# Optimization experiments

Hardware: AMD Instinct MI355X
Metric: run time of the kernel (lower is better)

The kernel has to match this reference:

```python
import jax, jax.numpy as jnp
import numpy as np

N = 100000

def gcn_conv(x, edge_index, W, b):
    # PyG GCNConv: add self-loops, symmetric norm D^-1/2 (A+I) D^-1/2, then aggregate x@W
    n = x.shape[0]
    loops = jnp.arange(n, dtype=edge_index.dtype)
    row = jnp.concatenate([edge_index[0], loops])  # source
    col = jnp.concatenate([edge_index[1], loops])  # target
    deg = jax.ops.segment_sum(jnp.ones_like(col, dtype=x.dtype), col, num_segments=n)
    dinv = jnp.where(deg > 0, jax.lax.rsqrt(deg), 0.0)
    norm = dinv[row] * dinv[col]            # [E+N]
    xw = x @ W                               # transform first (smaller message dim)
    msg = xw[row] * norm[:, None]            # gather + normalize
    out = jax.ops.segment_sum(msg, col, num_segments=n)  # scatter-add
    return out + b

def setup_inputs() -> dict:
    key = jax.random.key(0)
    k1, k2, k3, k4, k5, k6 = jax.random.split(key, 6)
    F_in, H, C = 512, 256, 40
    x = jax.random.normal(k1, (N, F_in), dtype=jnp.float32)
    edge_index = jax.random.randint(k2, (2, 3200000), 0, N, dtype=jnp.int64)
    W1 = jax.random.normal(k3, (F_in, H), dtype=jnp.float32) / np.sqrt(F_in)
    b1 = jnp.zeros((H,), dtype=jnp.float32)
    W2 = jax.random.normal(k4, (H, C), dtype=jnp.float32) / np.sqrt(H)
    b2 = jnp.zeros((C,), dtype=jnp.float32)
    return {"x": x, "edge_index": edge_index, "W1": W1, "b1": b1, "W2": W2, "b2": b2}

def reference(x, edge_index, W1, b1, W2, b2):
    h = gcn_conv(x, edge_index, W1, b1)
    h = jax.nn.relu(h)
    # dropout skipped (eval mode / training=False)
    h = gcn_conv(h, edge_index, W2, b2)
    return jax.nn.log_softmax(h, axis=1)
```

## Files before the change

kernel.cpp:

```cpp
#include <hip/hip_runtime.h>
#include <math.h>

typedef __attribute__((ext_vector_type(8))) short short8;
typedef __attribute__((ext_vector_type(4))) float f32x4;

typedef __attribute__((address_space(1))) const unsigned int guint;
typedef __attribute__((address_space(3))) unsigned int luint;

static __device__ __forceinline__ unsigned short f2bf(float f) {
    unsigned int u = __float_as_uint(f);
    unsigned int r = (u + 0x7FFFu + ((u >> 16) & 1u)) >> 16;
    return (unsigned short)r;
}
static __device__ __forceinline__ float b2f(unsigned short s) {
    return __uint_as_float(((unsigned int)s) << 16);
}


__global__ void count_kernel(const int* __restrict__ ei, int* __restrict__ cnt, int E) {
    int e = blockIdx.x * 256 + threadIdx.x;
    if (e < E) atomicAdd(&cnt[ei[E + e]], 1);
}

__global__ void scanA_kernel(const int* __restrict__ cnt, float* __restrict__ dinv,
                             int* __restrict__ colptr, int* __restrict__ bsum, int n) {
    __shared__ int s[256];
    int b = blockIdx.x, t = threadIdx.x;
    int i = b * 512 + 2 * t;
    int c0 = (i     < n) ? cnt[i]     : 0;
    int c1 = (i + 1 < n) ? cnt[i + 1] : 0;
    if (i     < n) dinv[i]     = rsqrtf((float)(c0 + 1));
    if (i + 1 < n) dinv[i + 1] = rsqrtf((float)(c1 + 1));
    int v = c0 + c1;
    s[t] = v;
    __syncthreads();
    #pragma unroll
    for (int o = 1; o < 256; o <<= 1) {
        int x = (t >= o) ? s[t - o] : 0;
        __syncthreads();
        s[t] += x;
        __syncthreads();
    }
    int excl = s[t] - v;
    if (i     < n) colptr[i]     = excl;
    if (i + 1 < n) colptr[i + 1] = excl + c0;
    if (t == 255) bsum[b] = s[t];
}

__global__ void scanB_kernel(int* bsum, int nb) {
    __shared__ int s[256];
    int t = threadIdx.x;
    int v = (t < nb) ? bsum[t] : 0;
    s[t] = v;
    __syncthreads();
    #pragma unroll
    for (int o = 1; o < 256; o <<= 1) {
        int x = (t >= o) ? s[t - o] : 0;
        __syncthreads();
        s[t] += x;
        __syncthreads();
    }
    if (t < nb) bsum[t] = s[t] - v;
}

__global__ void scanC_kernel(int* __restrict__ colptr, const int* __restrict__ bsum,
                             int n, int E) {
    int b = blockIdx.x, t = threadIdx.x;
    int off = bsum[b];
    int i = b * 512 + 2 * t;
    if (i     < n) colptr[i]     += off;
    if (i + 1 < n) colptr[i + 1] += off;
    if (b == 0 && t == 0) colptr[n] = E;
}

__global__ void fill_kernel(const int* __restrict__ ei, const int* __restrict__ colptr,
                            int* __restrict__ fillc, int* __restrict__ eidx, int E) {
    int e = blockIdx.x * 256 + threadIdx.x;
    if (e < E) {
        int r = ei[e];
        int c = ei[E + e];
        int pos = colptr[c] + atomicAdd(&fillc[c], 1);
        eidx[pos] = r;
    }
}


__global__ void convert_x_kernel(const float* __restrict__ x, unsigned short* __restrict__ xb,
                                 long valid, long total) {
    long off = ((long)blockIdx.x * 256 + threadIdx.x) * 4;
    if (off >= total) return;
    float4 v = make_float4(0.f, 0.f, 0.f, 0.f);
    if (off < valid) v = *(const float4*)(x + off);
    uint2 p;
    p.x = (unsigned int)f2bf(v.x) | ((unsigned int)f2bf(v.y) << 16);
    p.y = (unsigned int)f2bf(v.z) | ((unsigned int)f2bf(v.w) << 16);
    *(uint2*)(xb + off) = p;
}

__global__ void convert_w1_kernel(const float* __restrict__ W1, unsigned short* __restrict__ w1t) {
    int id = blockIdx.x * 256 + threadIdx.x;
    int k = id >> 8, n = id & 255;
    w1t[(size_t)n * 512 + k] = f2bf(W1[id]);
}


__global__ __launch_bounds__(256) void gemm1_kernel(const unsigned short* __restrict__ xb,
                                                    const unsigned short* __restrict__ w1t,
                                                    const float* __restrict__ dinv,
                                                    unsigned short* __restrict__ xs, int M) {
    __shared__ short As[128 * 32];
    __shared__ short Bs[128 * 32];
    int t = threadIdx.x;
    int m0 = blockIdx.x * 128, n0 = blockIdx.y * 128;
    int lane = t & 63, wv = t >> 6;
    int wm = (wv & 1) * 64, wn = (wv >> 1) * 64;
    int lm = lane & 15, q = lane >> 4;

    int am0 = t >> 2, ak = (t & 3) * 8;
    const unsigned short* Ag0 = xb  + (size_t)(m0 + am0) * 512 + ak;
    const unsigned short* Ag1 = xb  + (size_t)(m0 + am0 + 64) * 512 + ak;
    const unsigned short* Bg0 = w1t + (size_t)(n0 + am0) * 512 + ak;
    const unsigned short* Bg1 = w1t + (size_t)(n0 + am0 + 64) * 512 + ak;
    short* Al0 = As + t * 8;
    short* Al1 = As + t * 8 + 2048;
    short* Bl0 = Bs + t * 8;
    short* Bl1 = Bs + t * 8 + 2048;

    f32x4 acc[4][4];
    f32x4 z = {0.f, 0.f, 0.f, 0.f};
    #pragma unroll
    for (int i = 0; i < 4; i++)
        #pragma unroll
        for (int j = 0; j < 4; j++) acc[i][j] = z;

    for (int k0 = 0; k0 < 512; k0 += 32) {
        __syncthreads();
        __builtin_amdgcn_global_load_lds((guint*)(Ag0 + k0), (luint*)Al0, 16, 0, 0);
        __builtin_amdgcn_global_load_lds((guint*)(Ag1 + k0), (luint*)Al1, 16, 0, 0);
        __builtin_amdgcn_global_load_lds((guint*)(Bg0 + k0), (luint*)Bl0, 16, 0, 0);
        __builtin_amdgcn_global_load_lds((guint*)(Bg1 + k0), (luint*)Bl1, 16, 0, 0);
        __syncthreads();
        short8 af[4], bf[4];
        #pragma unroll
        for (int i = 0; i < 4; i++)
            af[i] = *(const short8*)(As + (wm + i * 16 + lm) * 32 + q * 8);
        #pragma unroll
        for (int j = 0; j < 4; j++)
            bf[j] = *(const short8*)(Bs + (wn + j * 16 + lm) * 32 + q * 8);
        #pragma unroll
        for (int i = 0; i < 4; i++)
            #pragma unroll
            for (int j = 0; j < 4; j++)
                acc[i][j] = __builtin_amdgcn_mfma_f32_16x16x32_bf16(af[i], bf[j], acc[i][j], 0, 0, 0);
    }

    #pragma unroll
    for (int i = 0; i < 4; i++) {
        #pragma unroll
        for (int r = 0; r < 4; r++) {
            int m = m0 + wm + i * 16 + q * 4 + r;
            if (m < M) {
                float d = dinv[m];
                #pragma unroll
                for (int j = 0; j < 4; j++) {
                    int n = n0 + wn + j * 16 + lm;
                    xs[(size_t)m * 256 + n] = f2bf(acc[i][j][r] * d);
                }
            }
        }
    }
}


__global__ __launch_bounds__(256) void spmm1_kernel(const unsigned short* __restrict__ xs,
                                                    const int* __restrict__ colptr,
                                                    const int* __restrict__ eidx,
                                                    const float* __restrict__ dinv,
                                                    const float* __restrict__ b1,
                                                    unsigned short* __restrict__ h, int Nn) {
    int wid = threadIdx.x >> 6, lane = threadIdx.x & 63;
    int c = blockIdx.x * 4 + wid;
    if (c >= Nn) return;
    const uint2* base = (const uint2*)xs;
    uint2 sv = base[(size_t)c * 64 + lane];
    float a0 = b2f((unsigned short)(sv.x & 0xFFFF));
    float a1 = __uint_as_float(sv.x & 0xFFFF0000u);
    float a2 = b2f((unsigned short)(sv.y & 0xFFFF));
    float a3 = __uint_as_float(sv.y & 0xFFFF0000u);
    int j = colptr[c], jend = colptr[c + 1];
    for (; j + 3 < jend; j += 4) {
        int r0 = eidx[j], r1 = eidx[j + 1], r2 = eidx[j + 2], r3 = eidx[j + 3];
        uint2 v0 = base[(size_t)r0 * 64 + lane];
        uint2 v1 = base[(size_t)r1 * 64 + lane];
        uint2 v2 = base[(size_t)r2 * 64 + lane];
        uint2 v3 = base[(size_t)r3 * 64 + lane];
        a0 += __uint_as_float(v0.x << 16) + __uint_as_float(v1.x << 16)
            + __uint_as_float(v2.x << 16) + __uint_as_float(v3.x << 16);
        a1 += __uint_as_float(v0.x & 0xFFFF0000u) + __uint_as_float(v1.x & 0xFFFF0000u)
            + __uint_as_float(v2.x & 0xFFFF0000u) + __uint_as_float(v3.x & 0xFFFF0000u);
        a2 += __uint_as_float(v0.y << 16) + __uint_as_float(v1.y << 16)
            + __uint_as_float(v2.y << 16) + __uint_as_float(v3.y << 16);
        a3 += __uint_as_float(v0.y & 0xFFFF0000u) + __uint_as_float(v1.y & 0xFFFF0000u)
            + __uint_as_float(v2.y & 0xFFFF0000u) + __uint_as_float(v3.y & 0xFFFF0000u);
    }
    for (; j < jend; j++) {
        uint2 v0 = base[(size_t)eidx[j] * 64 + lane];
        a0 += __uint_as_float(v0.x << 16);
        a1 += __uint_as_float(v0.x & 0xFFFF0000u);
        a2 += __uint_as_float(v0.y << 16);
        a3 += __uint_as_float(v0.y & 0xFFFF0000u);
    }
    float d = dinv[c];
    float4 bb = ((const float4*)b1)[lane];
    float f0 = fmaxf(a0 * d + bb.x, 0.f);
    float f1 = fmaxf(a1 * d + bb.y, 0.f);
    float f2 = fmaxf(a2 * d + bb.z, 0.f);
    float f3 = fmaxf(a3 * d + bb.w, 0.f);
    uint2 p;
    p.x = (unsigned int)f2bf(f0) | ((unsigned int)f2bf(f1) << 16);
    p.y = (unsigned int)f2bf(f2) | ((unsigned int)f2bf(f3) << 16);
    *(uint2*)(h + (size_t)c * 256 + 4 * lane) = p;
}


__global__ __launch_bounds__(320) void gemm2_kernel(const unsigned short* __restrict__ h,
                                                    const float* __restrict__ W2,
                                                    const float* __restrict__ dinv,
                                                    unsigned short* __restrict__ t2, int M) {
    __shared__ float w2s[256 * 40];
    __shared__ float hs[32][260];
    int t = threadIdx.x;
    for (int idx = t; idx < 10240; idx += 320) w2s[idx] = W2[idx];
    int r0g = blockIdx.x * 32;
    for (int idx = t; idx < 2048; idx += 320) {
        int rr = idx >> 6, k4 = (idx & 63) * 4;
        int row = r0g + rr;
        float4 v = make_float4(0.f, 0.f, 0.f, 0.f);
        if (row < M) {
            uint2 u = *(const uint2*)(h + (size_t)row * 256 + k4);
            v.x = __uint_as_float(u.x << 16);
            v.y = __uint_as_float(u.x & 0xFFFF0000u);
            v.z = __uint_as_float(u.y << 16);
            v.w = __uint_as_float(u.y & 0xFFFF0000u);
        }
        *(float4*)&hs[rr][k4] = v;
    }
    __syncthreads();
    int c = t % 40, rb = (t / 40) * 4;
    float a0 = 0.f, a1 = 0.f, a2 = 0.f, a3 = 0.f;
    #pragma unroll 2
    for (int k = 0; k < 256; k += 4) {
        float4 h0 = *(const float4*)&hs[rb + 0][k];
        float4 h1 = *(const float4*)&hs[rb + 1][k];
        float4 h2 = *(const float4*)&hs[rb + 2][k];
        float4 h3 = *(const float4*)&hs[rb + 3][k];
        float w0 = w2s[(k + 0) * 40 + c];
        float w1 = w2s[(k + 1) * 40 + c];
        float w2 = w2s[(k + 2) * 40 + c];
        float w3 = w2s[(k + 3) * 40 + c];
        a0 += h0.x * w0 + h0.y * w1 + h0.z * w2 + h0.w * w3;
        a1 += h1.x * w0 + h1.y * w1 + h1.z * w2 + h1.w * w3;
        a2 += h2.x * w0 + h2.y * w1 + h2.z * w2 + h2.w * w3;
        a3 += h3.x * w0 + h3.y * w1 + h3.z * w2 + h3.w * w3;
    }
    int row = r0g + rb;
    if (row + 0 < M) t2[(size_t)(row + 0) * 40 + c] = f2bf(a0 * dinv[row + 0]);
    if (row + 1 < M) t2[(size_t)(row + 1) * 40 + c] = f2bf(a1 * dinv[row + 1]);
    if (row + 2 < M) t2[(size_t)(row + 2) * 40 + c] = f2bf(a2 * dinv[row + 2]);
    if (row + 3 < M) t2[(size_t)(row + 3) * 40 + c] = f2bf(a3 * dinv[row + 3]);
}


__global__ __launch_bounds__(256) void spmm2_kernel(const unsigned short* __restrict__ t2,
                                                    const int* __restrict__ colptr,
                                                    const int* __restrict__ eidx,
                                                    const float* __restrict__ dinv,
                                                    const float* __restrict__ b2,
                                                    float* __restrict__ out, int Nn) {
    int wid = threadIdx.x >> 6, lane = threadIdx.x & 63;
    int c = blockIdx.x * 4 + wid;
    if (c >= Nn) return;
    int f = (lane < 40) ? lane : 0;
    float acc = b2f(t2[(size_t)c * 40 + f]);
    int j = colptr[c], jend = colptr[c + 1];
    float a0 = 0.f, a1 = 0.f, a2 = 0.f, a3 = 0.f;
    for (; j + 3 < jend; j += 4) {
        int r0 = eidx[j], r1 = eidx[j + 1], r2 = eidx[j + 2], r3 = eidx[j + 3];
        a0 += b2f(t2[(size_t)r0 * 40 + f]);
        a1 += b2f(t2[(size_t)r1 * 40 + f]);
        a2 += b2f(t2[(size_t)r2 * 40 + f]);
        a3 += b2f(t2[(size_t)r3 * 40 + f]);
    }
    for (; j < jend; j++) a0 += b2f(t2[(size_t)eidx[j] * 40 + f]);
    acc += (a0 + a1) + (a2 + a3);
    float val = (lane < 40) ? (acc * dinv[c] + b2[f]) : -INFINITY;
    float m = val;
    #pragma unroll
    for (int o = 32; o > 0; o >>= 1) { float z = __shfl_xor(m, o); m = fmaxf(m, z); }
    float ex = (lane < 40) ? expf(val - m) : 0.f;
    float s = ex;
    #pragma unroll
    for (int o = 32; o > 0; o >>= 1) s += __shfl_xor(s, o);
    if (lane < 40) out[(size_t)c * 40 + lane] = val - m - logf(s);
}


extern "C" void kernel_launch(void* const* d_in, const int* in_sizes, int n_in,
                              void* d_out, int out_size, void* d_ws, size_t ws_size,
                              hipStream_t stream) {
    const float* x  = (const float*)d_in[0];
    const int*   ei = (const int*)d_in[1];
    const float* W1 = (const float*)d_in[2];
    const float* b1 = (const float*)d_in[3];
    const float* W2 = (const float*)d_in[4];
    const float* b2 = (const float*)d_in[5];
    float* out = (float*)d_out;

    int N = in_sizes[0] / 512;
    int E = in_sizes[1] / 2;
    int Mpad = ((N + 127) / 128) * 128;

    char* p = (char*)d_ws;
    auto carve = [&](size_t bytes) -> char* {
        char* q = p;
        p += (bytes + 1023) & ~(size_t)1023;
        return q;
    };
    float* dinv   = (float*)carve((size_t)N * 4);
    int*   cnt    = (int*)carve((size_t)N * 4);
    int*   colptr = (int*)carve(((size_t)N + 1) * 4);
    int*   fillc  = (int*)carve((size_t)N * 4);
    int*   bsum   = (int*)carve(1024 * 4);
    int*   eidx   = (int*)carve((size_t)E * 4);
    unsigned short* w1t = (unsigned short*)carve((size_t)256 * 512 * 2);
    unsigned short* xb  = (unsigned short*)carve((size_t)Mpad * 512 * 2);
    unsigned short* xs  = (unsigned short*)carve((size_t)Mpad * 256 * 2);
    unsigned short* h  = xb;
    unsigned short* t2 = xb + (size_t)Mpad * 256;

    hipMemsetAsync(cnt,   0, (size_t)N * 4, stream);
    hipMemsetAsync(fillc, 0, (size_t)N * 4, stream);

    int eb = (E + 255) / 256;
    int nb = (N + 511) / 512;

    count_kernel<<<eb, 256, 0, stream>>>(ei, cnt, E);
    scanA_kernel<<<nb, 256, 0, stream>>>(cnt, dinv, colptr, bsum, N);
    scanB_kernel<<<1, 256, 0, stream>>>(bsum, nb);
    scanC_kernel<<<nb, 256, 0, stream>>>(colptr, bsum, N, E);
    fill_kernel<<<eb, 256, 0, stream>>>(ei, colptr, fillc, eidx, E);

    long totalx = (long)Mpad * 512;
    long validx = (long)N * 512;
    convert_x_kernel<<<(int)((totalx / 4 + 255) / 256), 256, 0, stream>>>(x, xb, validx, totalx);
    convert_w1_kernel<<<512, 256, 0, stream>>>(W1, w1t);

    dim3 g1(Mpad / 128, 2);
    gemm1_kernel<<<g1, 256, 0, stream>>>(xb, w1t, dinv, xs, N);
    spmm1_kernel<<<(N + 3) / 4, 256, 0, stream>>>(xs, colptr, eidx, dinv, b1, h, N);
    gemm2_kernel<<<(N + 31) / 32, 320, 0, stream>>>(h, W2, dinv, t2, N);
    spmm2_kernel<<<(N + 3) / 4, 256, 0, stream>>>(t2, colptr, eidx, dinv, b2, out, N);
}
```

Measured before the change: 1.089 ms.

## Fuse fp32-to-bf16 conversion of x into GEMM1 and pad layer-2 rows

```diff
diff --git a/kernel.cpp b/kernel.cpp
--- a/kernel.cpp
+++ b/kernel.cpp
@@ -3,9 +3,6 @@
 
 typedef __attribute__((ext_vector_type(8))) short short8;
 typedef __attribute__((ext_vector_type(4))) float f32x4;
-
-typedef __attribute__((address_space(1))) const unsigned int guint;
-typedef __attribute__((address_space(3))) unsigned int luint;
 
 static __device__ __forceinline__ unsigned short f2bf(float f) {
     unsigned int u = __float_as_uint(f);
@@ -84,19 +81,6 @@
     }
 }
 
-
-__global__ void convert_x_kernel(const float* __restrict__ x, unsigned short* __restrict__ xb,
-                                 long valid, long total) {
-    long off = ((long)blockIdx.x * 256 + threadIdx.x) * 4;
-    if (off >= total) return;
-    float4 v = make_float4(0.f, 0.f, 0.f, 0.f);
-    if (off < valid) v = *(const float4*)(x + off);
-    uint2 p;
-    p.x = (unsigned int)f2bf(v.x) | ((unsigned int)f2bf(v.y) << 16);
-    p.y = (unsigned int)f2bf(v.z) | ((unsigned int)f2bf(v.w) << 16);
-    *(uint2*)(xb + off) = p;
-}
-
 __global__ void convert_w1_kernel(const float* __restrict__ W1, unsigned short* __restrict__ w1t) {
     int id = blockIdx.x * 256 + threadIdx.x;
     int k = id >> 8, n = id & 255;
@@ -104,27 +88,22 @@
 }
 
 
-__global__ __launch_bounds__(256) void gemm1_kernel(const unsigned short* __restrict__ xb,
+__global__ __launch_bounds__(256) void gemm1_kernel(const float* __restrict__ x,
                                                     const unsigned short* __restrict__ w1t,
                                                     const float* __restrict__ dinv,
                                                     unsigned short* __restrict__ xs, int M) {
-    __shared__ short As[128 * 32];
-    __shared__ short Bs[128 * 32];
+    __shared__ unsigned short As[64 * 40];
+    __shared__ unsigned short Bs[256 * 40];
     int t = threadIdx.x;
-    int m0 = blockIdx.x * 128, n0 = blockIdx.y * 128;
+    int m0 = blockIdx.x * 64;
     int lane = t & 63, wv = t >> 6;
-    int wm = (wv & 1) * 64, wn = (wv >> 1) * 64;
+    int wn = wv * 64;
     int lm = lane & 15, q = lane >> 4;
 
-    int am0 = t >> 2, ak = (t & 3) * 8;
-    const unsigned short* Ag0 = xb  + (size_t)(m0 + am0) * 512 + ak;
-    const unsigned short* Ag1 = xb  + (size_t)(m0 + am0 + 64) * 512 + ak;
-    const unsigned short* Bg0 = w1t + (size_t)(n0 + am0) * 512 + ak;
-    const unsigned short* Bg1 = w1t + (size_t)(n0 + am0 + 64) * 512 + ak;
-    short* Al0 = As + t * 8;
-    short* Al1 = As + t * 8 + 2048;
-    short* Bl0 = Bs + t * 8;
-    short* Bl1 = Bs + t * 8 + 2048;
+    int ra = t >> 2, kc = (t & 3) * 8;
+    int am = m0 + ra; if (am >= M) am = M - 1;
+    const float* Ap = x + (size_t)am * 512 + kc;
+    const unsigned short* Bp = w1t + (size_t)ra * 512 + kc;
 
     f32x4 acc[4][4];
     f32x4 z = {0.f, 0.f, 0.f, 0.f};
@@ -134,36 +113,48 @@
         for (int j = 0; j < 4; j++) acc[i][j] = z;
 
     for (int k0 = 0; k0 < 512; k0 += 32) {
-        __syncthreads();
-        __builtin_amdgcn_global_load_lds((guint*)(Ag0 + k0), (luint*)Al0, 16, 0, 0);
-        __builtin_amdgcn_global_load_lds((guint*)(Ag1 + k0), (luint*)Al1, 16, 0, 0);
-        __builtin_amdgcn_global_load_lds((guint*)(Bg0 + k0), (luint*)Bl0, 16, 0, 0);
-        __builtin_amdgcn_global_load_lds((guint*)(Bg1 + k0), (luint*)Bl1, 16, 0, 0);
-        __syncthreads();
-        short8 af[4], bf[4];
+        float4 a0 = *(const float4*)(Ap + k0);
+        float4 a1 = *(const float4*)(Ap + k0 + 4);
+        uint4 b0 = *(const uint4*)(Bp + k0);
+        uint4 b1 = *(const uint4*)(Bp + k0 + 64 * 512);
+        uint4 b2 = *(const uint4*)(Bp + k0 + 128 * 512);
+        uint4 b3 = *(const uint4*)(Bp + k0 + 192 * 512);
+        __syncthreads();
+        uint4 ap;
+        ap.x = (unsigned int)f2bf(a0.x) | ((unsigned int)f2bf(a0.y) << 16);
+        ap.y = (unsigned int)f2bf(a0.z) | ((unsigned int)f2bf(a0.w) << 16);
+        ap.z = (unsigned int)f2bf(a1.x) | ((unsigned int)f2bf(a1.y) << 16);
+        ap.w = (unsigned int)f2bf(a1.z) | ((unsigned int)f2bf(a1.w) << 16);
+        *(uint4*)&As[ra * 40 + kc] = ap;
+        *(uint4*)&Bs[(ra +   0) * 40 + kc] = b0;
+        *(uint4*)&Bs[(ra +  64) * 40 + kc] = b1;
+        *(uint4*)&Bs[(ra + 128) * 40 + kc] = b2;
+        *(uint4*)&Bs[(ra + 192) * 40 + kc] = b3;
+        __syncthreads();
+        short8 af[4], bfr[4];
         #pragma unroll
         for (int i = 0; i < 4; i++)
-            af[i] = *(const short8*)(As + (wm + i * 16 + lm) * 32 + q * 8);
+            af[i] = *(const short8*)&As[(i * 16 + lm) * 40 + q * 8];
         #pragma unroll
         for (int j = 0; j < 4; j++)
-            bf[j] = *(const short8*)(Bs + (wn + j * 16 + lm) * 32 + q * 8);
+            bfr[j] = *(const short8*)&Bs[(wn + j * 16 + lm) * 40 + q * 8];
         #pragma unroll
         for (int i = 0; i < 4; i++)
             #pragma unroll
             for (int j = 0; j < 4; j++)
-                acc[i][j] = __builtin_amdgcn_mfma_f32_16x16x32_bf16(af[i], bf[j], acc[i][j], 0, 0, 0);
+                acc[i][j] = __builtin_amdgcn_mfma_f32_16x16x32_bf16(af[i], bfr[j], acc[i][j], 0, 0, 0);
     }
 
     #pragma unroll
     for (int i = 0; i < 4; i++) {
         #pragma unroll
         for (int r = 0; r < 4; r++) {
-            int m = m0 + wm + i * 16 + q * 4 + r;
+            int m = m0 + i * 16 + q * 4 + r;
             if (m < M) {
                 float d = dinv[m];
                 #pragma unroll
                 for (int j = 0; j < 4; j++) {
-                    int n = n0 + wn + j * 16 + lm;
+                    int n = wn + j * 16 + lm;
                     xs[(size_t)m * 256 + n] = f2bf(acc[i][j][r] * d);
                 }
             }
@@ -183,25 +174,36 @@
     if (c >= Nn) return;
     const uint2* base = (const uint2*)xs;
     uint2 sv = base[(size_t)c * 64 + lane];
-    float a0 = b2f((unsigned short)(sv.x & 0xFFFF));
+    float a0 = __uint_as_float(sv.x << 16);
     float a1 = __uint_as_float(sv.x & 0xFFFF0000u);
-    float a2 = b2f((unsigned short)(sv.y & 0xFFFF));
+    float a2 = __uint_as_float(sv.y << 16);
     float a3 = __uint_as_float(sv.y & 0xFFFF0000u);
     int j = colptr[c], jend = colptr[c + 1];
-    for (; j + 3 < jend; j += 4) {
-        int r0 = eidx[j], r1 = eidx[j + 1], r2 = eidx[j + 2], r3 = eidx[j + 3];
-        uint2 v0 = base[(size_t)r0 * 64 + lane];
-        uint2 v1 = base[(size_t)r1 * 64 + lane];
-        uint2 v2 = base[(size_t)r2 * 64 + lane];
-        uint2 v3 = base[(size_t)r3 * 64 + lane];
+    for (; j + 7 < jend; j += 8) {
+        uint2 v0 = base[(size_t)eidx[j    ] * 64 + lane];
+        uint2 v1 = base[(size_t)eidx[j + 1] * 64 + lane];
+        uint2 v2 = base[(size_t)eidx[j + 2] * 64 + lane];
+        uint2 v3 = base[(size_t)eidx[j + 3] * 64 + lane];
+        uint2 v4 = base[(size_t)eidx[j + 4] * 64 + lane];
+        uint2 v5 = base[(size_t)eidx[j + 5] * 64 + lane];
+        uint2 v6 = base[(size_t)eidx[j + 6] * 64 + lane];
+        uint2 v7 = base[(size_t)eidx[j + 7] * 64 + lane];
         a0 += __uint_as_float(v0.x << 16) + __uint_as_float(v1.x << 16)
-            + __uint_as_float(v2.x << 16) + __uint_as_float(v3.x << 16);
+            + __uint_as_float(v2.x << 16) + __uint_as_float(v3.x << 16)
+            + __uint_as_float(v4.x << 16) + __uint_as_float(v5.x << 16)
+            + __uint_as_float(v6.x << 16) + __uint_as_float(v7.x << 16);
         a1 += __uint_as_float(v0.x & 0xFFFF0000u) + __uint_as_float(v1.x & 0xFFFF0000u)
-            + __uint_as_float(v2.x & 0xFFFF0000u) + __uint_as_float(v3.x & 0xFFFF0000u);
+            + __uint_as_float(v2.x & 0xFFFF0000u) + __uint_as_float(v3.x & 0xFFFF0000u)
+            + __uint_as_float(v4.x & 0xFFFF0000u) + __uint_as_float(v5.x & 0xFFFF0000u)
+            + __uint_as_float(v6.x & 0xFFFF0000u) + __uint_as_float(v7.x & 0xFFFF0000u);
         a2 += __uint_as_float(v0.y << 16) + __uint_as_float(v1.y << 16)
-            + __uint_as_float(v2.y << 16) + __uint_as_float(v3.y << 16);
+            + __uint_as_float(v2.y << 16) + __uint_as_float(v3.y << 16)
+            + __uint_as_float(v4.y << 16) + __uint_as_float(v5.y << 16)
+            + __uint_as_float(v6.y << 16) + __uint_as_float(v7.y << 16);
         a3 += __uint_as_float(v0.y & 0xFFFF0000u) + __uint_as_float(v1.y & 0xFFFF0000u)
-            + __uint_as_float(v2.y & 0xFFFF0000u) + __uint_as_float(v3.y & 0xFFFF0000u);
+            + __uint_as_float(v2.y & 0xFFFF0000u) + __uint_as_float(v3.y & 0xFFFF0000u)
+            + __uint_as_float(v4.y & 0xFFFF0000u) + __uint_as_float(v5.y & 0xFFFF0000u)
+            + __uint_as_float(v6.y & 0xFFFF0000u) + __uint_as_float(v7.y & 0xFFFF0000u);
     }
     for (; j < jend; j++) {
         uint2 v0 = base[(size_t)eidx[j] * 64 + lane];
@@ -226,7 +228,7 @@
 __global__ __launch_bounds__(320) void gemm2_kernel(const unsigned short* __restrict__ h,
                                                     const float* __restrict__ W2,
                                                     const float* __restrict__ dinv,
-                                                    unsigned short* __restrict__ t2, int M) {
+                                                    unsigned short* __restrict__ t2p, int M) {
     __shared__ float w2s[256 * 40];
     __shared__ float hs[32][260];
     int t = threadIdx.x;
@@ -264,14 +266,14 @@
         a3 += h3.x * w0 + h3.y * w1 + h3.z * w2 + h3.w * w3;
     }
     int row = r0g + rb;
-    if (row + 0 < M) t2[(size_t)(row + 0) * 40 + c] = f2bf(a0 * dinv[row + 0]);
-    if (row + 1 < M) t2[(size_t)(row + 1) * 40 + c] = f2bf(a1 * dinv[row + 1]);
-    if (row + 2 < M) t2[(size_t)(row + 2) * 40 + c] = f2bf(a2 * dinv[row + 2]);
-    if (row + 3 < M) t2[(size_t)(row + 3) * 40 + c] = f2bf(a3 * dinv[row + 3]);
-}
-
-
-__global__ __launch_bounds__(256) void spmm2_kernel(const unsigned short* __restrict__ t2,
+    if (row + 0 < M) t2p[(size_t)(row + 0) * 64 + c] = f2bf(a0 * dinv[row + 0]);
+    if (row + 1 < M) t2p[(size_t)(row + 1) * 64 + c] = f2bf(a1 * dinv[row + 1]);
+    if (row + 2 < M) t2p[(size_t)(row + 2) * 64 + c] = f2bf(a2 * dinv[row + 2]);
+    if (row + 3 < M) t2p[(size_t)(row + 3) * 64 + c] = f2bf(a3 * dinv[row + 3]);
+}
+
+
+__global__ __launch_bounds__(256) void spmm2_kernel(const unsigned short* __restrict__ t2p,
                                                     const int* __restrict__ colptr,
                                                     const int* __restrict__ eidx,
                                                     const float* __restrict__ dinv,
@@ -280,20 +282,23 @@
     int wid = threadIdx.x >> 6, lane = threadIdx.x & 63;
     int c = blockIdx.x * 4 + wid;
     if (c >= Nn) return;
-    int f = (lane < 40) ? lane : 0;
-    float acc = b2f(t2[(size_t)c * 40 + f]);
+    float acc = b2f(t2p[(size_t)c * 64 + lane]);
     int j = colptr[c], jend = colptr[c + 1];
     float a0 = 0.f, a1 = 0.f, a2 = 0.f, a3 = 0.f;
-    for (; j + 3 < jend; j += 4) {
-        int r0 = eidx[j], r1 = eidx[j + 1], r2 = eidx[j + 2], r3 = eidx[j + 3];
-        a0 += b2f(t2[(size_t)r0 * 40 + f]);
-        a1 += b2f(t2[(size_t)r1 * 40 + f]);
-        a2 += b2f(t2[(size_t)r2 * 40 + f]);
-        a3 += b2f(t2[(size_t)r3 * 40 + f]);
-    }
-    for (; j < jend; j++) a0 += b2f(t2[(size_t)eidx[j] * 40 + f]);
+    for (; j + 7 < jend; j += 8) {
+        float u0 = b2f(t2p[(size_t)eidx[j    ] * 64 + lane]);
+        float u1 = b2f(t2p[(size_t)eidx[j + 1] * 64 + lane]);
+        float u2 = b2f(t2p[(size_t)eidx[j + 2] * 64 + lane]);
+        float u3 = b2f(t2p[(size_t)eidx[j + 3] * 64 + lane]);
+        float u4 = b2f(t2p[(size_t)eidx[j + 4] * 64 + lane]);
+        float u5 = b2f(t2p[(size_t)eidx[j + 5] * 64 + lane]);
+        float u6 = b2f(t2p[(size_t)eidx[j + 6] * 64 + lane]);
+        float u7 = b2f(t2p[(size_t)eidx[j + 7] * 64 + lane]);
+        a0 += u0 + u4; a1 += u1 + u5; a2 += u2 + u6; a3 += u3 + u7;
+    }
+    for (; j < jend; j++) a0 += b2f(t2p[(size_t)eidx[j] * 64 + lane]);
     acc += (a0 + a1) + (a2 + a3);
-    float val = (lane < 40) ? (acc * dinv[c] + b2[f]) : -INFINITY;
+    float val = (lane < 40) ? (acc * dinv[c] + b2[lane]) : -INFINITY;
     float m = val;
     #pragma unroll
     for (int o = 32; o > 0; o >>= 1) { float z = __shfl_xor(m, o); m = fmaxf(m, z); }
@@ -318,7 +323,6 @@
 
     int N = in_sizes[0] / 512;
     int E = in_sizes[1] / 2;
-    int Mpad = ((N + 127) / 128) * 128;
 
     char* p = (char*)d_ws;
     auto carve = [&](size_t bytes) -> char* {
@@ -333,10 +337,9 @@
     int*   bsum   = (int*)carve(1024 * 4);
     int*   eidx   = (int*)carve((size_t)E * 4);
     unsigned short* w1t = (unsigned short*)carve((size_t)256 * 512 * 2);
-    unsigned short* xb  = (unsigned short*)carve((size_t)Mpad * 512 * 2);
-    unsigned short* xs  = (unsigned short*)carve((size_t)Mpad * 256 * 2);
-    unsigned short* h  = xb;
-    unsigned short* t2 = xb + (size_t)Mpad * 256;
+    unsigned short* xs  = (unsigned short*)carve((size_t)N * 256 * 2);
+    unsigned short* h   = (unsigned short*)carve((size_t)N * 256 * 2);
+    unsigned short* t2p = (unsigned short*)carve((size_t)N * 64 * 2);
 
     hipMemsetAsync(cnt,   0, (size_t)N * 4, stream);
     hipMemsetAsync(fillc, 0, (size_t)N * 4, stream);
@@ -349,15 +352,11 @@
     scanB_kernel<<<1, 256, 0, stream>>>(bsum, nb);
     scanC_kernel<<<nb, 256, 0, stream>>>(colptr, bsum, N, E);
     fill_kernel<<<eb, 256, 0, stream>>>(ei, colptr, fillc, eidx, E);
-
-    long totalx = (long)Mpad * 512;
-    long validx = (long)N * 512;
-    convert_x_kernel<<<(int)((totalx / 4 + 255) / 256), 256, 0, stream>>>(x, xb, validx, totalx);
     convert_w1_kernel<<<512, 256, 0, stream>>>(W1, w1t);
 
-    dim3 g1(Mpad / 128, 2);
-    gemm1_kernel<<<g1, 256, 0, stream>>>(xb, w1t, dinv, xs, N);
+    int mb = (N + 63) / 64;
+    gemm1_kernel<<<mb, 256, 0, stream>>>(x, w1t, dinv, xs, N);
     spmm1_kernel<<<(N + 3) / 4, 256, 0, stream>>>(xs, colptr, eidx, dinv, b1, h, N);
-    gemm2_kernel<<<(N + 31) / 32, 320, 0, stream>>>(h, W2, dinv, t2, N);
-    spmm2_kernel<<<(N + 3) / 4, 256, 0, stream>>>(t2, colptr, eidx, dinv, b2, out, N);
-}
+    gemm2_kernel<<<(N + 31) / 32, 320, 0, stream>>>(h, W2, dinv, t2p, N);
+    spmm2_kernel<<<(N + 3) / 4, 256, 0, stream>>>(t2p, colptr, eidx, dinv, b2, out, N);
+}
```

Result: faster. 1.050 ms (-3.5%).
